# Kernel tuning notes

Hardware: AMD Instinct MI355X
Metric: run time of the kernel (lower is better)

Reference implementation:

```python
import jax, jax.numpy as jnp
import numpy as np
from math import pi

H = 1024        # hidden_size
CAP = 32        # capacity (even -> CAP//2 even+odd rotation pairs)
EH = H // 2         # even_hidden_size = 512
OH = (H - 1) // 2   # odd_hidden_size  = 511
PAIRS = CAP // 2    # 16

# fixed permutations (hidden_size even branch of the original module)
_PE = np.arange(H).reshape(-1, 2)[:, ::-1].reshape(-1)                       # swap (0,1),(2,3),...
_inner = np.arange(1, 2 * OH + 1).reshape(-1, 2)[:, ::-1].reshape(-1)
_PO = np.concatenate([[0], _inner, [2 * OH + 1]])                            # fix ends, swap interior pairs


def cm(x, y):
    """complex multiply; real/imag stacked in last dim."""
    xr, xi = x[..., 0], x[..., 1]
    yr, yi = y[..., 0], y[..., 1]
    return jnp.stack([xr * yr - xi * yi, xr * yi + xi * yr], -1)


def _ilv(a, b):
    """interleave two [n] vectors -> [2n]."""
    return jnp.stack([a, b], 1).reshape(-1)


def setup_inputs() -> dict:
    key = jax.random.key(0)
    ks = jax.random.split(key, 6)
    u = lambda k, shape: jax.random.uniform(k, shape, jnp.float32) * (2 * pi) - pi
    return {
        "x": jax.random.normal(ks[0], (4096, H, 2), jnp.float32),
        "omega": u(ks[1], (H,)),
        "even_theta": u(ks[2], (PAIRS, EH)),
        "odd_theta": u(ks[3], (PAIRS, OH)),
        "even_phi": u(ks[4], (PAIRS, EH)),
        "odd_phi": u(ks[5], (PAIRS, OH)),
    }


def reference(x, omega, even_theta, odd_theta, even_phi, odd_phi):
    PE = jnp.asarray(_PE)
    PO = jnp.asarray(_PO)

    def step(xc, p):
        et, ep, ot, op = p
        # ---- even rotation (note: original code swaps cos_phi/sin_phi in the
        # call to _v_diag/_v_off_diag; replicated faithfully here) ----
        ct, st, cp, sp = jnp.cos(et), jnp.sin(et), jnp.cos(ep), jnp.sin(ep)
        z = jnp.zeros_like(ct)
        vd = jnp.stack([_ilv(sp * ct, ct), _ilv(cp * ct, z)], -1)          # [H,2]
        vo = jnp.stack([_ilv(-sp * st, st), _ilv(-cp * st, z)], -1)        # [H,2]
        xc = cm(xc, vd) + cm(xc[:, PE, :], vo)
        # ---- odd rotation (ends padded with identity) ----
        ct, st, cp, sp = jnp.cos(ot), jnp.sin(ot), jnp.cos(op), jnp.sin(op)
        z = jnp.zeros_like(ct)
        one = jnp.ones((1,), xc.dtype)
        zero = jnp.zeros((1,), xc.dtype)
        vd_re = jnp.concatenate([one, _ilv(sp * ct, ct), one])
        vd_im = jnp.concatenate([zero, _ilv(cp * ct, z), zero])
        vo_re = jnp.concatenate([zero, _ilv(-sp * st, st), zero])
        vo_im = jnp.concatenate([zero, _ilv(-cp * st, z), zero])
        xc = cm(xc, jnp.stack([vd_re, vd_im], -1)) + cm(xc[:, PO, :], jnp.stack([vo_re, vo_im], -1))
        return xc, None

    x, _ = jax.lax.scan(step, x, (even_theta, even_phi, odd_theta, odd_phi))
    # final diagonal phase
    x = cm(x, jnp.stack([jnp.cos(omega), jnp.sin(omega)], -1))
    return x
```

## Files before the change

kernel.cpp:

```cpp
#include <hip/hip_runtime.h>
#include <math.h>


typedef float f4 __attribute__((ext_vector_type(4)));

#define OMCS_OFF 65536

__global__ __launch_bounds__(256) void eunn_precompute(
    const float* __restrict__ omega, const float* __restrict__ et,
    const float* __restrict__ ot, const float* __restrict__ ep,
    const float* __restrict__ op, float* __restrict__ ws) {
  int tid = blockIdx.x * 256 + threadIdx.x;
  if (tid < 16384) {
    int s = tid >> 10, k = tid & 1023;
    int phase = k >> 9, j = k & 511;
    float ct, st, cp, sp;
    if (phase == 0) {
      sincosf(et[s * 512 + j], &st, &ct);
      sincosf(ep[s * 512 + j], &sp, &cp);
    } else if (j < 511) {
      sincosf(ot[s * 511 + j], &st, &ct);
      sincosf(op[s * 511 + j], &sp, &cp);
    } else {
      ct = 1.f; st = 0.f; cp = 0.f; sp = 1.f;
    }
    ((f4*)ws)[s * 1024 + phase * 512 + (j & 7) * 64 + (j >> 3)] =
        (f4){ct, st, cp, sp};
  } else if (tid < 16896) {
    int m = tid - 16384;
    float s0, c0, s1, c1;
    sincosf(omega[2 * m], &s0, &c0);
    sincosf(omega[2 * m + 1], &s1, &c1);
    ((f4*)(ws + OMCS_OFF))[(m & 7) * 64 + (m >> 3)] = (f4){c0, s0, c1, s1};
  }
}

template <int R>
__global__ __launch_bounds__(256, 2) void eunn_main(
    const float* __restrict__ x, float* __restrict__ out,
    const float* __restrict__ ws) {
  const int lane = threadIdx.x & 63;
  const int wid = blockIdx.x * (blockDim.x >> 6) + (threadIdx.x >> 6);
  const f4* cf = (const f4*)ws + lane;

  f4 e[R][8];
#pragma unroll
  for (int r = 0; r < R; ++r) {
    const f4* xr = (const f4*)(x + (size_t)(wid * R + r) * 2048) + lane * 8;
#pragma unroll
    for (int p = 0; p < 8; ++p) e[r][p] = xr[p];
  }

  f4 E[8];
#pragma unroll
  for (int p = 0; p < 8; ++p) E[p] = cf[p * 64];

#pragma unroll 1
  for (int s = 0; s < 16; ++s) {
    f4 O[8];
    {
      const f4* ob = cf + s * 1024 + 512;
#pragma unroll
      for (int p = 0; p < 8; ++p) O[p] = ob[p * 64];
    }
#pragma unroll
    for (int r = 0; r < R; ++r) {
#pragma unroll
      for (int p = 0; p < 8; ++p) {
        f4 c = E[p];
        f4 v = e[r][p];
        float t0 = c.x * v.x - c.y * v.z;
        float t1 = c.x * v.y - c.y * v.w;
        e[r][p] = (f4){c.w * t0 - c.z * t1, c.z * t0 + c.w * t1,
                       c.y * v.x + c.x * v.z, c.y * v.y + c.x * v.w};
      }
    }
    {
      const f4* nb = cf + ((s + 1) & 15) * 1024;
#pragma unroll
      for (int p = 0; p < 8; ++p) E[p] = nb[p * 64];
    }
    {
      float ctm = __shfl_up(O[7].x, 1, 64);
      float stm = __shfl_up(O[7].y, 1, 64);
      if (lane == 0) { ctm = 1.f; stm = 0.f; }
#pragma unroll
      for (int r = 0; r < R; ++r) {
        float upx = __shfl_down(e[r][0].x, 1, 64);
        float upy = __shfl_down(e[r][0].y, 1, 64);
        float dnz = __shfl_up(e[r][7].z, 1, 64);
        float dnw = __shfl_up(e[r][7].w, 1, 64);
        float nx = stm * dnz + ctm * e[r][0].x;
        float ny = stm * dnw + ctm * e[r][0].y;
        e[r][0].x = nx;
        e[r][0].y = ny;
#pragma unroll
        for (int p = 0; p < 7; ++p) {
          f4 c = O[p];
          float e0r = e[r][p].z, e0i = e[r][p].w;
          float e1r = e[r][p + 1].x, e1i = e[r][p + 1].y;
          float t0 = c.x * e0r - c.y * e1r;
          float t1 = c.x * e0i - c.y * e1i;
          e[r][p].z = c.w * t0 - c.z * t1;
          e[r][p].w = c.z * t0 + c.w * t1;
          e[r][p + 1].x = c.y * e0r + c.x * e1r;
          e[r][p + 1].y = c.y * e0i + c.x * e1i;
        }
        {
          f4 c = O[7];
          float e0r = e[r][7].z, e0i = e[r][7].w;
          float t0 = c.x * e0r - c.y * upx;
          float t1 = c.x * e0i - c.y * upy;
          e[r][7].z = c.w * t0 - c.z * t1;
          e[r][7].w = c.z * t0 + c.w * t1;
        }
      }
    }
  }

  const f4* om4 = (const f4*)(ws + OMCS_OFF) + lane;
#pragma unroll
  for (int r = 0; r < R; ++r) {
    f4* outr = (f4*)(out + (size_t)(wid * R + r) * 2048) + lane * 8;
#pragma unroll
    for (int p = 0; p < 8; ++p) {
      f4 v = e[r][p];
      f4 w = om4[p * 64];
      outr[p] = (f4){v.x * w.x - v.y * w.y, v.x * w.y + v.y * w.x,
                     v.z * w.z - v.w * w.w, v.z * w.w + v.w * w.z};
    }
  }
}

extern "C" void kernel_launch(void* const* d_in, const int* in_sizes, int n_in,
                              void* d_out, int out_size, void* d_ws, size_t ws_size,
                              hipStream_t stream) {
  const float* x     = (const float*)d_in[0];
  const float* omega = (const float*)d_in[1];
  const float* et    = (const float*)d_in[2];
  const float* ot    = (const float*)d_in[3];
  const float* ep    = (const float*)d_in[4];
  const float* op    = (const float*)d_in[5];
  float* out = (float*)d_out;
  float* ws  = (float*)d_ws;

  eunn_precompute<<<dim3(66), dim3(256), 0, stream>>>(omega, et, ot, ep, op, ws);

  eunn_main<2><<<dim3(512), dim3(256), 0, stream>>>(x, out, ws);
}
```

Before: 127.7 us.

## Stage per-step rotation coefficients into double-buffered LDS via async global loads

Each wave used to load its even and odd rotation coefficients straight from global memory every step. Now the block's four waves cooperatively stream each step's coefficient block into shared memory with global_load_lds, double-buffered so the next step's load overlaps the current step's compute. All waves then read the coefficients from LDS. This cuts redundant global and L2 traffic, at the cost of a block-wide barrier per step and 32KB of LDS per block.

Result: slower. 142.0 us (+11.1%).

```diff
diff --git a/kernel.cpp b/kernel.cpp
--- a/kernel.cpp
+++ b/kernel.cpp
@@ -40,8 +40,22 @@
     const float* __restrict__ x, float* __restrict__ out,
     const float* __restrict__ ws) {
   const int lane = threadIdx.x & 63;
-  const int wid = blockIdx.x * (blockDim.x >> 6) + (threadIdx.x >> 6);
-  const f4* cf = (const f4*)ws + lane;
+  const int wave = threadIdx.x >> 6;
+  const int wid = blockIdx.x * 4 + wave;
+
+  __shared__ f4 sbuf[2][1024];
+
+  auto stage = [&](int s2, f4* dst) {
+    const float* g = ws + s2 * 4096 + wave * 1024 + lane * 4;
+    char* lbase = (char*)dst + wave * 4096;
+#pragma unroll
+    for (int c = 0; c < 4; ++c) {
+      __builtin_amdgcn_global_load_lds(
+          (const __attribute__((address_space(1))) void*)(g + c * 256),
+          (__attribute__((address_space(3))) void*)(lbase + c * 1024),
+          16, 0, 0);
+    }
+  };
 
   f4 e[R][8];
 #pragma unroll
@@ -51,18 +65,17 @@
     for (int p = 0; p < 8; ++p) e[r][p] = xr[p];
   }
 
-  f4 E[8];
-#pragma unroll
-  for (int p = 0; p < 8; ++p) E[p] = cf[p * 64];
+  f4* rd = sbuf[0];
+  f4* wr = sbuf[1];
+  stage(0, rd);
 
 #pragma unroll 1
   for (int s = 0; s < 16; ++s) {
-    f4 O[8];
-    {
-      const f4* ob = cf + s * 1024 + 512;
+    __syncthreads();
+    if (s < 15) stage(s + 1, wr);
+    f4 E[8];
 #pragma unroll
-      for (int p = 0; p < 8; ++p) O[p] = ob[p * 64];
-    }
+    for (int p = 0; p < 8; ++p) E[p] = rd[p * 64 + lane];
 #pragma unroll
     for (int r = 0; r < R; ++r) {
 #pragma unroll
@@ -75,11 +88,9 @@
                        c.y * v.x + c.x * v.z, c.y * v.y + c.x * v.w};
       }
     }
-    {
-      const f4* nb = cf + ((s + 1) & 15) * 1024;
+    f4 O[8];
 #pragma unroll
-      for (int p = 0; p < 8; ++p) E[p] = nb[p * 64];
-    }
+    for (int p = 0; p < 8; ++p) O[p] = rd[512 + p * 64 + lane];
     {
       float ctm = __shfl_up(O[7].x, 1, 64);
       float stm = __shfl_up(O[7].y, 1, 64);
@@ -116,6 +127,7 @@
         }
       }
     }
+    f4* t = rd; rd = wr; wr = t;
   }
 
   const f4* om4 = (const f4*)(ws + OMCS_OFF) + lane;
```

## Store rotation coefficients in fp16 and use one row per wave

Applied to the files above, without the earlier changes.

The precomputed cos/sin coefficient table is now stored as half-precision vectors, which halves the coefficient load traffic each step. The main kernel drops the two-rows-per-wave template and processes one row per wave, with double the blocks and a higher occupancy hint in launch bounds. This is meant to cut per-step coefficient bandwidth and register pressure to allow more waves per CU. It costs fp16 rounding of the rotation coefficients, which accumulates over 32 rotations and may break accuracy tolerance, and coefficient loads are no longer amortized across two rows.

Result: slower. 134.5 us (+5.3%).

```diff
diff --git a/kernel.cpp b/kernel.cpp
--- a/kernel.cpp
+++ b/kernel.cpp
@@ -3,8 +3,9 @@
 
 
 typedef float f4 __attribute__((ext_vector_type(4)));
+typedef _Float16 h4 __attribute__((ext_vector_type(4)));
 
-#define OMCS_OFF 65536
+#define OMCS_OFF 32768
 
 __global__ __launch_bounds__(256) void eunn_precompute(
     const float* __restrict__ omega, const float* __restrict__ et,
@@ -24,8 +25,8 @@
     } else {
       ct = 1.f; st = 0.f; cp = 0.f; sp = 1.f;
     }
-    ((f4*)ws)[s * 1024 + phase * 512 + (j & 7) * 64 + (j >> 3)] =
-        (f4){ct, st, cp, sp};
+    ((h4*)ws)[s * 1024 + phase * 512 + (j & 7) * 64 + (j >> 3)] =
+        (h4){(_Float16)ct, (_Float16)st, (_Float16)cp, (_Float16)sp};
   } else if (tid < 16896) {
     int m = tid - 16384;
     float s0, c0, s1, c1;
@@ -35,96 +36,90 @@
   }
 }
 
-template <int R>
-__global__ __launch_bounds__(256, 2) void eunn_main(
+__global__ __launch_bounds__(256, 4) void eunn_main(
     const float* __restrict__ x, float* __restrict__ out,
     const float* __restrict__ ws) {
   const int lane = threadIdx.x & 63;
-  const int wid = blockIdx.x * (blockDim.x >> 6) + (threadIdx.x >> 6);
-  const f4* cf = (const f4*)ws + lane;
+  const int wid = blockIdx.x * 4 + (threadIdx.x >> 6);
+  const h4* cf = (const h4*)ws + lane;
 
-  f4 e[R][8];
+  f4 e[8];
+  {
+    const f4* xr = (const f4*)(x + (size_t)wid * 2048) + lane * 8;
 #pragma unroll
-  for (int r = 0; r < R; ++r) {
-    const f4* xr = (const f4*)(x + (size_t)(wid * R + r) * 2048) + lane * 8;
-#pragma unroll
-    for (int p = 0; p < 8; ++p) e[r][p] = xr[p];
+    for (int p = 0; p < 8; ++p) e[p] = xr[p];
   }
 
-  f4 E[8];
+  h4 E[8];
 #pragma unroll
   for (int p = 0; p < 8; ++p) E[p] = cf[p * 64];
 
 #pragma unroll 1
   for (int s = 0; s < 16; ++s) {
-    f4 O[8];
+    h4 O[8];
     {
-      const f4* ob = cf + s * 1024 + 512;
+      const h4* ob = cf + s * 1024 + 512;
 #pragma unroll
       for (int p = 0; p < 8; ++p) O[p] = ob[p * 64];
     }
 #pragma unroll
-    for (int r = 0; r < R; ++r) {
-#pragma unroll
-      for (int p = 0; p < 8; ++p) {
-        f4 c = E[p];
-        f4 v = e[r][p];
-        float t0 = c.x * v.x - c.y * v.z;
-        float t1 = c.x * v.y - c.y * v.w;
-        e[r][p] = (f4){c.w * t0 - c.z * t1, c.z * t0 + c.w * t1,
-                       c.y * v.x + c.x * v.z, c.y * v.y + c.x * v.w};
-      }
+    for (int p = 0; p < 8; ++p) {
+      h4 c = E[p];
+      float cx = (float)c.x, cy = (float)c.y, cz = (float)c.z, cw = (float)c.w;
+      f4 v = e[p];
+      float t0 = cx * v.x - cy * v.z;
+      float t1 = cx * v.y - cy * v.w;
+      e[p] = (f4){cw * t0 - cz * t1, cz * t0 + cw * t1,
+                  cy * v.x + cx * v.z, cy * v.y + cx * v.w};
     }
     {
-      const f4* nb = cf + ((s + 1) & 15) * 1024;
+      const h4* nb = cf + ((s + 1) & 15) * 1024;
 #pragma unroll
       for (int p = 0; p < 8; ++p) E[p] = nb[p * 64];
     }
     {
-      float ctm = __shfl_up(O[7].x, 1, 64);
-      float stm = __shfl_up(O[7].y, 1, 64);
+      float ctm = __shfl_up((float)O[7].x, 1, 64);
+      float stm = __shfl_up((float)O[7].y, 1, 64);
       if (lane == 0) { ctm = 1.f; stm = 0.f; }
+      float upx = __shfl_down(e[0].x, 1, 64);
+      float upy = __shfl_down(e[0].y, 1, 64);
+      float dnz = __shfl_up(e[7].z, 1, 64);
+      float dnw = __shfl_up(e[7].w, 1, 64);
+      float nx = stm * dnz + ctm * e[0].x;
+      float ny = stm * dnw + ctm * e[0].y;
+      e[0].x = nx;
+      e[0].y = ny;
 #pragma unroll
-      for (int r = 0; r < R; ++r) {
-        float upx = __shfl_down(e[r][0].x, 1, 64);
-        float upy = __shfl_down(e[r][0].y, 1, 64);
-        float dnz = __shfl_up(e[r][7].z, 1, 64);
-        float dnw = __shfl_up(e[r][7].w, 1, 64);
-        float nx = stm * dnz + ctm * e[r][0].x;
-        float ny = stm * dnw + ctm * e[r][0].y;
-        e[r][0].x = nx;
-        e[r][0].y = ny;
-#pragma unroll
-        for (int p = 0; p < 7; ++p) {
-          f4 c = O[p];
-          float e0r = e[r][p].z, e0i = e[r][p].w;
-          float e1r = e[r][p + 1].x, e1i = e[r][p + 1].y;
-          float t0 = c.x * e0r - c.y * e1r;
-          float t1 = c.x * e0i - c.y * e1i;
-          e[r][p].z = c.w * t0 - c.z * t1;
-          e[r][p].w = c.z * t0 + c.w * t1;
-          e[r][p + 1].x = c.y * e0r + c.x * e1r;
-          e[r][p + 1].y = c.y * e0i + c.x * e1i;
-        }
-        {
-          f4 c = O[7];
-          float e0r = e[r][7].z, e0i = e[r][7].w;
-          float t0 = c.x * e0r - c.y * upx;
-          float t1 = c.x * e0i - c.y * upy;
-          e[r][7].z = c.w * t0 - c.z * t1;
-          e[r][7].w = c.z * t0 + c.w * t1;
-        }
+      for (int p = 0; p < 7; ++p) {
+        h4 c = O[p];
+        float cx = (float)c.x, cy = (float)c.y, cz = (float)c.z, cw = (float)c.w;
+        float e0r = e[p].z, e0i = e[p].w;
+        float e1r = e[p + 1].x, e1i = e[p + 1].y;
+        float t0 = cx * e0r - cy * e1r;
+        float t1 = cx * e0i - cy * e1i;
+        e[p].z = cw * t0 - cz * t1;
+        e[p].w = cz * t0 + cw * t1;
+        e[p + 1].x = cy * e0r + cx * e1r;
+        e[p + 1].y = cy * e0i + cx * e1i;
+      }
+      {
+        h4 c = O[7];
+        float cx = (float)c.x, cy = (float)c.y, cz = (float)c.z, cw = (float)c.w;
+        float e0r = e[7].z, e0i = e[7].w;
+        float t0 = cx * e0r - cy * upx;
+        float t1 = cx * e0i - cy * upy;
+        e[7].z = cw * t0 - cz * t1;
+        e[7].w = cz * t0 + cw * t1;
       }
     }
   }
 
   const f4* om4 = (const f4*)(ws + OMCS_OFF) + lane;
-#pragma unroll
-  for (int r = 0; r < R; ++r) {
-    f4* outr = (f4*)(out + (size_t)(wid * R + r) * 2048) + lane * 8;
+  {
+    f4* outr = (f4*)(out + (size_t)wid * 2048) + lane * 8;
 #pragma unroll
     for (int p = 0; p < 8; ++p) {
-      f4 v = e[r][p];
+      f4 v = e[p];
       f4 w = om4[p * 64];
       outr[p] = (f4){v.x * w.x - v.y * w.y, v.x * w.y + v.y * w.x,
                      v.z * w.z - v.w * w.w, v.z * w.w + v.w * w.z};
@@ -146,5 +141,5 @@
 
   eunn_precompute<<<dim3(66), dim3(256), 0, stream>>>(omega, et, ot, ep, op, ws);
 
-  eunn_main<2><<<dim3(512), dim3(256), 0, stream>>>(x, out, ws);
+  eunn_main<<<dim3(1024), dim3(256), 0, stream>>>(x, out, ws);
 }
```

## Stage rotation coefficients in LDS via async double-buffered global_load_lds

Applied to the files above, without the earlier changes.

Each block now copies the precomputed per-stage rotation coefficients into shared memory with async global-to-LDS loads, double-buffering pairs of stages so the next group loads while the current one is computed. Each wave handles one row instead of two, and blocks grow to 512 threads to keep total work coverage the same. This replaces per-wave redundant global/L2 reads of the coefficients with one shared copy per block, and the cross-lane coefficient shuffle becomes an LDS read. The cost is 64KB of LDS per block and a block-wide barrier per stage pair, which could limit occupancy and reduces per-thread instruction-level parallelism.

After: 144.5 us. +13.1%, slower.

```diff
diff --git a/kernel.cpp b/kernel.cpp
--- a/kernel.cpp
+++ b/kernel.cpp
@@ -3,6 +3,7 @@
 
 
 typedef float f4 __attribute__((ext_vector_type(4)));
+typedef float f2 __attribute__((ext_vector_type(2)));
 
 #define OMCS_OFF 65536
 
@@ -35,96 +36,107 @@
   }
 }
 
-template <int R>
-__global__ __launch_bounds__(256, 2) void eunn_main(
+__global__ __launch_bounds__(512, 2) void eunn_main(
     const float* __restrict__ x, float* __restrict__ out,
     const float* __restrict__ ws) {
   const int lane = threadIdx.x & 63;
-  const int wid = blockIdx.x * (blockDim.x >> 6) + (threadIdx.x >> 6);
-  const f4* cf = (const f4*)ws + lane;
+  const int wid = blockIdx.x * 8 + (threadIdx.x >> 6);
 
-  f4 e[R][8];
+  __shared__ __attribute__((aligned(16))) f4 lds[4096];
+
+  {
+    const char* src = (const char*)ws + threadIdx.x * 16;
+    char* dst = (char*)lds + threadIdx.x * 16;
 #pragma unroll
-  for (int r = 0; r < R; ++r) {
-    const f4* xr = (const f4*)(x + (size_t)(wid * R + r) * 2048) + lane * 8;
-#pragma unroll
-    for (int p = 0; p < 8; ++p) e[r][p] = xr[p];
+    for (int r = 0; r < 4; ++r) {
+      __builtin_amdgcn_global_load_lds(
+          (const __attribute__((address_space(1))) void*)(src + r * 8192),
+          (__attribute__((address_space(3))) void*)(dst + r * 8192), 16, 0, 0);
+    }
   }
 
-  f4 E[8];
+  f4 e[8];
+  {
+    const f4* xr = (const f4*)(x + (size_t)wid * 2048) + lane * 8;
 #pragma unroll
-  for (int p = 0; p < 8; ++p) E[p] = cf[p * 64];
+    for (int p = 0; p < 8; ++p) e[p] = xr[p];
+  }
+
+  __syncthreads();
 
 #pragma unroll 1
-  for (int s = 0; s < 16; ++s) {
-    f4 O[8];
-    {
-      const f4* ob = cf + s * 1024 + 512;
+  for (int g = 0; g < 8; ++g) {
+    if (g < 7) {
+      const char* src = (const char*)ws + (g + 1) * 32768 + threadIdx.x * 16;
+      char* dst = (char*)lds + ((g + 1) & 1) * 32768 + threadIdx.x * 16;
 #pragma unroll
-      for (int p = 0; p < 8; ++p) O[p] = ob[p * 64];
+      for (int r = 0; r < 4; ++r) {
+        __builtin_amdgcn_global_load_lds(
+            (const __attribute__((address_space(1))) void*)(src + r * 8192),
+            (__attribute__((address_space(3))) void*)(dst + r * 8192), 16, 0,
+            0);
+      }
     }
+    const f4* B = lds + (g & 1) * 2048;
 #pragma unroll
-    for (int r = 0; r < R; ++r) {
+    for (int k = 0; k < 2; ++k) {
+      const f4* L = B + k * 1024;
+      f4 E[8];
+#pragma unroll
+      for (int p = 0; p < 8; ++p) E[p] = L[p * 64 + lane];
 #pragma unroll
       for (int p = 0; p < 8; ++p) {
         f4 c = E[p];
-        f4 v = e[r][p];
+        f4 v = e[p];
         float t0 = c.x * v.x - c.y * v.z;
         float t1 = c.x * v.y - c.y * v.w;
-        e[r][p] = (f4){c.w * t0 - c.z * t1, c.z * t0 + c.w * t1,
-                       c.y * v.x + c.x * v.z, c.y * v.y + c.x * v.w};
+        e[p] = (f4){c.w * t0 - c.z * t1, c.z * t0 + c.w * t1,
+                    c.y * v.x + c.x * v.z, c.y * v.y + c.x * v.w};
       }
-    }
-    {
-      const f4* nb = cf + ((s + 1) & 15) * 1024;
+      f4 O[8];
 #pragma unroll
-      for (int p = 0; p < 8; ++p) E[p] = nb[p * 64];
-    }
-    {
-      float ctm = __shfl_up(O[7].x, 1, 64);
-      float stm = __shfl_up(O[7].y, 1, 64);
-      if (lane == 0) { ctm = 1.f; stm = 0.f; }
-#pragma unroll
-      for (int r = 0; r < R; ++r) {
-        float upx = __shfl_down(e[r][0].x, 1, 64);
-        float upy = __shfl_down(e[r][0].y, 1, 64);
-        float dnz = __shfl_up(e[r][7].z, 1, 64);
-        float dnw = __shfl_up(e[r][7].w, 1, 64);
-        float nx = stm * dnz + ctm * e[r][0].x;
-        float ny = stm * dnw + ctm * e[r][0].y;
-        e[r][0].x = nx;
-        e[r][0].y = ny;
+      for (int p = 0; p < 8; ++p) O[p] = L[512 + p * 64 + lane];
+      f2 cm = ((const f2*)L)[(512 + 7 * 64 + ((lane + 63) & 63)) * 2];
+      {
+        float upx = __shfl_down(e[0].x, 1, 64);
+        float upy = __shfl_down(e[0].y, 1, 64);
+        float dnz = __shfl_up(e[7].z, 1, 64);
+        float dnw = __shfl_up(e[7].w, 1, 64);
+        float nx = cm.y * dnz + cm.x * e[0].x;
+        float ny = cm.y * dnw + cm.x * e[0].y;
+        e[0].x = nx;
+        e[0].y = ny;
 #pragma unroll
         for (int p = 0; p < 7; ++p) {
           f4 c = O[p];
-          float e0r = e[r][p].z, e0i = e[r][p].w;
-          float e1r = e[r][p + 1].x, e1i = e[r][p + 1].y;
+          float e0r = e[p].z, e0i = e[p].w;
+          float e1r = e[p + 1].x, e1i = e[p + 1].y;
           float t0 = c.x * e0r - c.y * e1r;
           float t1 = c.x * e0i - c.y * e1i;
-          e[r][p].z = c.w * t0 - c.z * t1;
-          e[r][p].w = c.z * t0 + c.w * t1;
-          e[r][p + 1].x = c.y * e0r + c.x * e1r;
-          e[r][p + 1].y = c.y * e0i + c.x * e1i;
+          e[p].z = c.w * t0 - c.z * t1;
+          e[p].w = c.z * t0 + c.w * t1;
+          e[p + 1].x = c.y * e0r + c.x * e1r;
+          e[p + 1].y = c.y * e0i + c.x * e1i;
         }
         {
           f4 c = O[7];
-          float e0r = e[r][7].z, e0i = e[r][7].w;
+          float e0r = e[7].z, e0i = e[7].w;
           float t0 = c.x * e0r - c.y * upx;
           float t1 = c.x * e0i - c.y * upy;
-          e[r][7].z = c.w * t0 - c.z * t1;
-          e[r][7].w = c.z * t0 + c.w * t1;
+          e[7].z = c.w * t0 - c.z * t1;
+          e[7].w = c.z * t0 + c.w * t1;
         }
       }
     }
+    __syncthreads();
   }
 
   const f4* om4 = (const f4*)(ws + OMCS_OFF) + lane;
-#pragma unroll
-  for (int r = 0; r < R; ++r) {
-    f4* outr = (f4*)(out + (size_t)(wid * R + r) * 2048) + lane * 8;
+  {
+    f4* outr = (f4*)(out + (size_t)wid * 2048) + lane * 8;
 #pragma unroll
     for (int p = 0; p < 8; ++p) {
-      f4 v = e[r][p];
+      f4 v = e[p];
       f4 w = om4[p * 64];
       outr[p] = (f4){v.x * w.x - v.y * w.y, v.x * w.y + v.y * w.x,
                      v.z * w.z - v.w * w.w, v.z * w.w + v.w * w.z};
@@ -146,5 +158,5 @@
 
   eunn_precompute<<<dim3(66), dim3(256), 0, stream>>>(omega, et, ot, ep, op, ws);
 
-  eunn_main<2><<<dim3(512), dim3(256), 0, stream>>>(x, out, ws);
+  eunn_main<<<dim3(512), dim3(512), 0, stream>>>(x, out, ws);
 }
```
